# Kernel tuning notes

Hardware: AMD Instinct MI355X
Metric: run time of the kernel (lower is better)

The kernel has to match this reference:

```python
import jax, jax.numpy as jnp
import numpy as np

NUM_CUSTOMERS = 300000
NUM_PRODUCTS = 150000
NUM_GROUPS = 2000
NUM_BRANDS = 500
EMB_DIM = 64
NUM_LAYERS = 3


def setup_inputs() -> dict:
    key = jax.random.key(0)
    ks = jax.random.split(key, 20)
    def ri(k, n, hi):
        return jax.random.randint(k, (n,), 0, hi, dtype=jnp.int32)
    return {
        'cust_w': 0.1 * jax.random.normal(ks[0], (NUM_CUSTOMERS, EMB_DIM), jnp.float32),
        'prod_w': 0.1 * jax.random.normal(ks[1], (NUM_PRODUCTS, EMB_DIM), jnp.float32),
        'group_w': 0.1 * jax.random.normal(ks[2], (NUM_GROUPS, EMB_DIM), jnp.float32),
        'brand_w': 0.1 * jax.random.normal(ks[3], (NUM_BRANDS, EMB_DIM), jnp.float32),
        'purch_src': ri(ks[4], 2000000, NUM_CUSTOMERS),
        'purch_dst': ri(ks[5], 2000000, NUM_PRODUCTS),
        'pby_src': ri(ks[6], 2000000, NUM_PRODUCTS),
        'pby_dst': ri(ks[7], 2000000, NUM_CUSTOMERS),
        'sim_src': ri(ks[8], 500000, NUM_PRODUCTS),
        'sim_dst': ri(ks[9], 500000, NUM_PRODUCTS),
        'cop_src': ri(ks[10], 1000000, NUM_PRODUCTS),
        'cop_dst': ri(ks[11], 1000000, NUM_PRODUCTS),
        'bel_src': ri(ks[12], 150000, NUM_PRODUCTS),
        'bel_dst': ri(ks[13], 150000, NUM_GROUPS),
        'comp_src': ri(ks[14], 300000, NUM_PRODUCTS),
        'comp_dst': ri(ks[15], 300000, NUM_BRANDS),
    }


def _propagate(src_idx, tgt_idx, tgt_emb, n_src):
    # gather target embeddings along edges, scatter-add into source buckets,
    # normalize by source out-degree (clamped to >= 1) -- LightGCN mean-agg.
    msg = tgt_emb[tgt_idx]                                    # [E, D]
    agg = jax.ops.segment_sum(msg, src_idx, num_segments=n_src)
    cnt = jax.ops.segment_sum(jnp.ones(src_idx.shape, tgt_emb.dtype),
                              src_idx, num_segments=n_src)
    return agg / jnp.maximum(cnt, 1.0)[:, None]


def reference(cust_w, prod_w, group_w, brand_w,
              purch_src, purch_dst, pby_src, pby_dst,
              sim_src, sim_dst, cop_src, cop_dst,
              bel_src, bel_dst, comp_src, comp_dst):
    customer_emb, product_emb = cust_w, prod_w
    group_emb, brand_emb = group_w, brand_w
    customer_embs = [customer_emb]
    product_embs = [product_emb]
    for _ in range(NUM_LAYERS):
        customer_to_product = _propagate(purch_src, purch_dst, product_emb, NUM_CUSTOMERS)
        product_agg = product_emb
        product_agg = product_agg + _propagate(pby_src, pby_dst, customer_emb, NUM_PRODUCTS)
        product_agg = product_agg + 0.5 * _propagate(sim_src, sim_dst, product_emb, NUM_PRODUCTS)
        product_agg = product_agg + 0.3 * _propagate(cop_src, cop_dst, product_emb, NUM_PRODUCTS)
        product_agg = product_agg + 0.2 * _propagate(bel_src, bel_dst, group_emb, NUM_PRODUCTS)
        product_agg = product_agg + 0.2 * _propagate(comp_src, comp_dst, brand_emb, NUM_PRODUCTS)
        customer_emb = customer_to_product
        product_emb = product_agg
        customer_embs.append(customer_emb)
        product_embs.append(product_emb)
    final_customer = jnp.mean(jnp.stack(customer_embs, 0), axis=0)
    final_product = jnp.mean(jnp.stack(product_embs, 0), axis=0)
    # group/brand embeddings are never updated -> mean of identical copies
    return (final_customer, final_product, group_emb, brand_emb)
```

## Files before the change

kernel.cpp:

```cpp
#include <hip/hip_runtime.h>

#define NC 300000
#define NP 150000
#define NG 2000
#define NB 500
#define SCAN_B 1024
#define BK_SHIFT 11
#define BK_KEYS 2048
#define NBKT 513
#define CH 8192

typedef unsigned int u32;
typedef float  f32x4 __attribute__((ext_vector_type(4)));
typedef unsigned int u32x4 __attribute__((ext_vector_type(4)));

static inline unsigned cdiv(long long a, long long b) { return (unsigned)((a + b - 1) / b); }

__device__ __forceinline__ float b2f(u32 h) {
    union { u32 u; float f; } c; c.u = h << 16; return c.f;
}
__device__ __forceinline__ u32 f2b(float f) {
    union { float f; u32 u; } c; c.f = f;
    return (c.u + 0x7FFFu + ((c.u >> 16) & 1u)) >> 16;
}
__device__ __forceinline__ void unpack8(uint4 v, float* o) {
    o[0] = b2f(v.x & 0xFFFFu); o[1] = b2f(v.x >> 16);
    o[2] = b2f(v.y & 0xFFFFu); o[3] = b2f(v.y >> 16);
    o[4] = b2f(v.z & 0xFFFFu); o[5] = b2f(v.z >> 16);
    o[6] = b2f(v.w & 0xFFFFu); o[7] = b2f(v.w >> 16);
}
__device__ __forceinline__ void unpack8v(u32x4 v, float* o) {
    o[0] = b2f(v.x & 0xFFFFu); o[1] = b2f(v.x >> 16);
    o[2] = b2f(v.y & 0xFFFFu); o[3] = b2f(v.y >> 16);
    o[4] = b2f(v.z & 0xFFFFu); o[5] = b2f(v.z >> 16);
    o[6] = b2f(v.w & 0xFFFFu); o[7] = b2f(v.w >> 16);
}
__device__ __forceinline__ uint4 pack8(const float* a) {
    uint4 v;
    v.x = f2b(a[0]) | (f2b(a[1]) << 16);
    v.y = f2b(a[2]) | (f2b(a[3]) << 16);
    v.z = f2b(a[4]) | (f2b(a[5]) << 16);
    v.w = f2b(a[6]) | (f2b(a[7]) << 16);
    return v;
}

__global__ void convert_all(const float* __restrict__ cw, const float* __restrict__ pw,
                            const float* __restrict__ gw, const float* __restrict__ bw,
                            uint4* __restrict__ c16, uint4* __restrict__ p16,
                            uint4* __restrict__ g16, uint4* __restrict__ b16,
                            float* __restrict__ outg, float* __restrict__ outb) {
    const int C8 = NC * 8, P8 = NP * 8, G8 = NG * 8, B8 = NB * 8;
    int i = blockIdx.x * blockDim.x + threadIdx.x;
    const float* in; uint4* out16; float* cpy = nullptr; int j;
    if (i < C8)                         { in = cw; out16 = c16; j = i; }
    else if ((j = i - C8) < P8)         { in = pw; out16 = p16; }
    else if ((j = i - C8 - P8) < G8)    { in = gw; out16 = g16; cpy = outg; }
    else if ((j = i - C8 - P8 - G8) < B8){ in = bw; out16 = b16; cpy = outb; }
    else return;
    const float4* p = (const float4*)(in + (size_t)j * 8);
    float4 a = p[0], b = p[1];
    float t[8] = { a.x, a.y, a.z, a.w, b.x, b.y, b.z, b.w };
    out16[j] = pack8(t);
    if (cpy) { float4* q = (float4*)(cpy + (size_t)j * 8); q[0] = a; q[1] = b; }
}

struct Edges6 {
    const int* src[6];
    const int* dst[6];
    int cum[7];
    int ctbase[7];
};

__global__ void bcount(Edges6 e, int* __restrict__ gcount, int total) {
    __shared__ int hist[NBKT];
    int t = threadIdx.x;
    int j0 = blockIdx.x * CH;
    for (int b = t; b < NBKT; b += blockDim.x) hist[b] = 0;
    __syncthreads();
    #pragma unroll 4
    for (int q = 0; q < CH / 256; ++q) {
        int j = j0 + q * 256 + t;
        if (j < total) {
            int k = 0;
            #pragma unroll
            for (int qq = 1; qq < 6; ++qq) k += (j >= e.cum[qq]);
            int key = e.ctbase[k] + __builtin_nontemporal_load(e.src[k] + (j - e.cum[k]));
            atomicAdd(&hist[key >> BK_SHIFT], 1);
        }
    }
    __syncthreads();
    for (int b = t; b < NBKT; b += blockDim.x) {
        int c = hist[b];
        if (c > 0) atomicAdd(gcount + b, c);
    }
}

__global__ void bscan(const int* __restrict__ gcount, int* __restrict__ gbase,
                      int* __restrict__ gcur, int nb) {
    __shared__ int sm[SCAN_B];
    int t = threadIdx.x;
    int v = (t < nb) ? gcount[t] : 0;
    sm[t] = v; __syncthreads();
    for (int off = 1; off < SCAN_B; off <<= 1) {
        int add = (t >= off) ? sm[t - off] : 0;
        __syncthreads();
        sm[t] += add; __syncthreads();
    }
    int excl = sm[t] - v;
    if (t < nb) { gbase[t] = excl; gcur[t] = excl; }
    if (t == nb - 1) gbase[nb] = sm[t];
}

__global__ void msplit(Edges6 e, int* __restrict__ gcur, u32* __restrict__ stage, int total) {
    __shared__ int hist[NBKT];
    __shared__ int bse[NBKT];
    int t = threadIdx.x;
    int j0 = blockIdx.x * CH;
    for (int b = t; b < NBKT; b += blockDim.x) hist[b] = 0;
    __syncthreads();
    #pragma unroll 4
    for (int q = 0; q < CH / 256; ++q) {
        int j = j0 + q * 256 + t;
        if (j < total) {
            int k = 0;
            #pragma unroll
            for (int qq = 1; qq < 6; ++qq) k += (j >= e.cum[qq]);
            int key = e.ctbase[k] + __builtin_nontemporal_load(e.src[k] + (j - e.cum[k]));
            atomicAdd(&hist[key >> BK_SHIFT], 1);
        }
    }
    __syncthreads();
    for (int b = t; b < NBKT; b += blockDim.x) {
        int c = hist[b];
        bse[b] = (c > 0) ? atomicAdd(gcur + b, c) : 0;
        hist[b] = 0;
    }
    __syncthreads();
    #pragma unroll 4
    for (int q = 0; q < CH / 256; ++q) {
        int j = j0 + q * 256 + t;
        if (j < total) {
            int k = 0;
            #pragma unroll
            for (int qq = 1; qq < 6; ++qq) k += (j >= e.cum[qq]);
            int jj = j - e.cum[k];
            int key = e.ctbase[k] + __builtin_nontemporal_load(e.src[k] + jj);
            int d = __builtin_nontemporal_load(e.dst[k] + jj);
            int b = key >> BK_SHIFT;
            int off = atomicAdd(&hist[b], 1);
            stage[bse[b] + off] = ((u32)(key & (BK_KEYS - 1)) << 19) | (u32)d;
        }
    }
}

__global__ void sortb(const int* __restrict__ gbase, const u32* __restrict__ stage,
                      int* __restrict__ pm, int* __restrict__ rp, int rtot) {
    __shared__ int cur[BK_KEYS];
    __shared__ int part[512];
    int b = blockIdx.x, t = threadIdx.x;
    int k0 = b << BK_SHIFT;
    int base = gbase[b], end = gbase[b + 1];
    for (int q = t; q < BK_KEYS; q += 512) cur[q] = 0;
    __syncthreads();
    for (int i = base + t; i < end; i += 512)
        atomicAdd(&cur[stage[i] >> 19], 1);
    __syncthreads();
    int a0 = cur[4 * t], a1 = cur[4 * t + 1], a2 = cur[4 * t + 2], a3 = cur[4 * t + 3];
    int s = a0 + a1 + a2 + a3;
    part[t] = s; __syncthreads();
    for (int off = 1; off < 512; off <<= 1) {
        int add = (t >= off) ? part[t - off] : 0;
        __syncthreads();
        part[t] += add; __syncthreads();
    }
    int c0 = base + part[t] - s;
    int c1 = c0 + a0, c2 = c1 + a1, c3 = c2 + a2;
    cur[4 * t] = c0; cur[4 * t + 1] = c1; cur[4 * t + 2] = c2; cur[4 * t + 3] = c3;
    int ki = k0 + 4 * t;
    if (ki + 3 < rtot) {
        *(int4*)(rp + ki) = make_int4(c0, c1, c2, c3);
    } else {
        if (ki     < rtot) rp[ki]     = c0;
        if (ki + 1 < rtot) rp[ki + 1] = c1;
        if (ki + 2 < rtot) rp[ki + 2] = c2;
        if (ki + 3 < rtot) rp[ki + 3] = c3;
    }
    __syncthreads();
    for (int i = base + t; i < end; i += 512) {
        u32 w = stage[i];
        int off = atomicAdd(&cur[w >> 19], 1);
        pm[off] = (int)(w & 0x7FFFFu);
    }
}

__device__ __forceinline__ void acc8(uint4 v, float* sum) {
    float t[8]; unpack8(v, t);
    #pragma unroll
    for (int k = 0; k < 8; ++k) sum[k] += t[k];
}
__device__ __forceinline__ void agg8se(int s, int e, const int* __restrict__ pm,
                                       const uint4* __restrict__ tgt,
                                       int lane, float w, float* acc) {
    float sum[8] = {0, 0, 0, 0, 0, 0, 0, 0};
    int i = s;
    for (; i + 4 <= e; i += 4) {
        int d0 = __builtin_nontemporal_load(pm + i);
        int d1 = __builtin_nontemporal_load(pm + i + 1);
        int d2 = __builtin_nontemporal_load(pm + i + 2);
        int d3 = __builtin_nontemporal_load(pm + i + 3);
        uint4 v0 = tgt[(size_t)d0 * 8 + lane];
        uint4 v1 = tgt[(size_t)d1 * 8 + lane];
        uint4 v2 = tgt[(size_t)d2 * 8 + lane];
        uint4 v3 = tgt[(size_t)d3 * 8 + lane];
        acc8(v0, sum); acc8(v1, sum); acc8(v2, sum); acc8(v3, sum);
    }
    for (; i < e; ++i) {
        int d = __builtin_nontemporal_load(pm + i);
        uint4 v = tgt[(size_t)d * 8 + lane];
        acc8(v, sum);
    }
    int deg = e - s;
    float sc = w / (float)(deg > 1 ? deg : 1);
    #pragma unroll
    for (int k = 0; k < 8; ++k) acc[k] += sum[k] * sc;
}

__global__ void layer_kernel(
    const int* __restrict__ rp_purch, const int* __restrict__ rp_pby,
    const int* __restrict__ rp_sim,   const int* __restrict__ rp_cop,
    const int* __restrict__ rp_bel,   const int* __restrict__ rp_comp,
    const int* __restrict__ pm,
    const uint4* __restrict__ c16, const uint4* __restrict__ p16,
    const uint4* __restrict__ g16, const uint4* __restrict__ b16,
    uint4* __restrict__ c16n, uint4* __restrict__ p16n,
    const float* __restrict__ cw, const float* __restrict__ pw,
    const uint4* __restrict__ s1c, const uint4* __restrict__ s1p,
    float* __restrict__ outc, float* __restrict__ outp,
    int mode)
{
    int t = blockIdx.x * blockDim.x + threadIdx.x;
    int gid = t >> 3;
    int lane = t & 7;
    float acc[8];
    if (gid < NP) {
        int row = gid;
        size_t idx = (size_t)row * 8 + lane;
        int s0 = rp_pby[row],  e0 = rp_pby[row + 1];
        int s1 = rp_sim[row],  e1 = rp_sim[row + 1];
        int s2 = rp_cop[row],  e2 = rp_cop[row + 1];
        int s3 = rp_bel[row],  e3 = rp_bel[row + 1];
        int s4 = rp_comp[row], e4 = rp_comp[row + 1];
        float base[8]; unpack8(p16[idx], base);
        #pragma unroll
        for (int k = 0; k < 8; ++k) acc[k] = base[k];
        agg8se(s0, e0, pm, c16, lane, 1.0f, acc);
        agg8se(s1, e1, pm, p16, lane, 0.5f, acc);
        agg8se(s2, e2, pm, p16, lane, 0.3f, acc);
        agg8se(s3, e3, pm, g16, lane, 0.2f, acc);
        agg8se(s4, e4, pm, b16, lane, 0.2f, acc);
        if (mode != 2) {
            p16n[idx] = pack8(acc);
        } else {
            const f32x4* s0p = (const f32x4*)(pw + (size_t)row * 64 + lane * 8);
            f32x4 a0 = __builtin_nontemporal_load(s0p);
            f32x4 a1 = __builtin_nontemporal_load(s0p + 1);
            u32x4 s1v = __builtin_nontemporal_load((const u32x4*)&s1p[idx]);
            float sv[8]; unpack8v(s1v, sv);
            f32x4 o0, o1;
            o0.x = 0.25f * (a0.x + sv[0] + base[0] + acc[0]);
            o0.y = 0.25f * (a0.y + sv[1] + base[1] + acc[1]);
            o0.z = 0.25f * (a0.z + sv[2] + base[2] + acc[2]);
            o0.w = 0.25f * (a0.w + sv[3] + base[3] + acc[3]);
            o1.x = 0.25f * (a1.x + sv[4] + base[4] + acc[4]);
            o1.y = 0.25f * (a1.y + sv[5] + base[5] + acc[5]);
            o1.z = 0.25f * (a1.z + sv[6] + base[6] + acc[6]);
            o1.w = 0.25f * (a1.w + sv[7] + base[7] + acc[7]);
            f32x4* o = (f32x4*)(outp + (size_t)row * 64 + lane * 8);
            __builtin_nontemporal_store(o0, o);
            __builtin_nontemporal_store(o1, o + 1);
        }
    } else if (gid < NP + NC) {
        int row = gid - NP;
        size_t idx = (size_t)row * 8 + lane;
        int s0 = rp_purch[row], e0 = rp_purch[row + 1];
        #pragma unroll
        for (int k = 0; k < 8; ++k) acc[k] = 0.f;
        agg8se(s0, e0, pm, p16, lane, 1.0f, acc);
        if (mode != 2) {
            c16n[idx] = pack8(acc);
        } else {
            float base[8]; unpack8(c16[idx], base);
            const f32x4* s0c = (const f32x4*)(cw + (size_t)row * 64 + lane * 8);
            f32x4 a0 = __builtin_nontemporal_load(s0c);
            f32x4 a1 = __builtin_nontemporal_load(s0c + 1);
            u32x4 s1v = __builtin_nontemporal_load((const u32x4*)&s1c[idx]);
            float sv[8]; unpack8v(s1v, sv);
            f32x4 o0, o1;
            o0.x = 0.25f * (a0.x + sv[0] + base[0] + acc[0]);
            o0.y = 0.25f * (a0.y + sv[1] + base[1] + acc[1]);
            o0.z = 0.25f * (a0.z + sv[2] + base[2] + acc[2]);
            o0.w = 0.25f * (a0.w + sv[3] + base[3] + acc[3]);
            o1.x = 0.25f * (a1.x + sv[4] + base[4] + acc[4]);
            o1.y = 0.25f * (a1.y + sv[5] + base[5] + acc[5]);
            o1.z = 0.25f * (a1.z + sv[6] + base[6] + acc[6]);
            o1.w = 0.25f * (a1.w + sv[7] + base[7] + acc[7]);
            f32x4* o = (f32x4*)(outc + (size_t)row * 64 + lane * 8);
            __builtin_nontemporal_store(o0, o);
            __builtin_nontemporal_store(o1, o + 1);
        }
    }
}

extern "C" void kernel_launch(void* const* d_in, const int* in_sizes, int n_in,
                              void* d_out, int out_size, void* d_ws, size_t ws_size,
                              hipStream_t stream) {
    const float* cust_w  = (const float*)d_in[0];
    const float* prod_w  = (const float*)d_in[1];
    const float* group_w = (const float*)d_in[2];
    const float* brand_w = (const float*)d_in[3];

    const int n_purch = in_sizes[4];
    const int n_pby   = in_sizes[6];
    const int n_sim   = in_sizes[8];
    const int n_cop   = in_sizes[10];
    const int n_bel   = in_sizes[12];
    const int n_comp  = in_sizes[14];
    const int n_edges[6] = { n_purch, n_pby, n_sim, n_cop, n_bel, n_comp };

    const size_t CSZ = (size_t)NC * 64;
    const size_t PSZ = (size_t)NP * 64;

    char* base = (char*)d_ws;
    uint4* c16A = (uint4*)base;                 base += (size_t)NC * 128;
    uint4* c16B = (uint4*)base;                 base += (size_t)NC * 128;
    uint4* p16A = (uint4*)base;                 base += (size_t)NP * 128;
    uint4* p16B = (uint4*)base;                 base += (size_t)NP * 128;
    uint4* g16  = (uint4*)base;                 base += (size_t)NG * 128;
    uint4* b16  = (uint4*)base;                 base += (size_t)NB * 128;

    const int RP_PURCH = NC + 1;
    const int RP_OTHER = NP + 1;
    const int RTOT = RP_PURCH + 5 * RP_OTHER;

    int* rp_all = (int*)base;                   base += (size_t)RTOT * 4;
    long long tot_edges = 0;
    for (int k = 0; k < 6; ++k) tot_edges += n_edges[k];
    int* pm_all = (int*)base;                   base += tot_edges * 4;
    u32* stage  = (u32*)base;                   base += tot_edges * 4;
    int* gcount = (int*)base;                   base += (size_t)NBKT * 4;
    int* gbase  = (int*)base;                   base += (size_t)(NBKT + 1) * 4;
    int* gcur   = (int*)base;

    int* rp_purch = rp_all;
    int* rp_pby   = rp_purch + RP_PURCH;
    int* rp_sim   = rp_pby + RP_OTHER;
    int* rp_cop   = rp_sim + RP_OTHER;
    int* rp_bel   = rp_cop + RP_OTHER;
    int* rp_comp  = rp_bel + RP_OTHER;

    float* out_c = (float*)d_out;
    float* out_p = out_c + CSZ;
    float* out_g = out_p + PSZ;
    float* out_b = out_g + (size_t)NG * 64;

    const int BT = 256;

    const long long CVT = (long long)(NC + NP + NG + NB) * 8;
    convert_all<<<cdiv(CVT, BT), BT, 0, stream>>>(
        cust_w, prod_w, group_w, brand_w, c16A, p16A, g16, b16, out_g, out_b);

    Edges6 E;
    E.src[0] = (const int*)d_in[4];  E.dst[0] = (const int*)d_in[5];
    E.src[1] = (const int*)d_in[6];  E.dst[1] = (const int*)d_in[7];
    E.src[2] = (const int*)d_in[8];  E.dst[2] = (const int*)d_in[9];
    E.src[3] = (const int*)d_in[10]; E.dst[3] = (const int*)d_in[11];
    E.src[4] = (const int*)d_in[12]; E.dst[4] = (const int*)d_in[13];
    E.src[5] = (const int*)d_in[14]; E.dst[5] = (const int*)d_in[15];
    E.cum[0] = 0;
    for (int k = 0; k < 6; ++k) E.cum[k + 1] = E.cum[k] + n_edges[k];
    E.ctbase[0] = 0;
    E.ctbase[1] = RP_PURCH;
    for (int k = 2; k < 6; ++k) E.ctbase[k] = E.ctbase[k - 1] + RP_OTHER;
    E.ctbase[6] = RTOT;
    const int TOT = E.cum[6];

    hipMemsetAsync(gcount, 0, (size_t)NBKT * 4, stream);
    bcount<<<cdiv(TOT, CH), BT, 0, stream>>>(E, gcount, TOT);
    bscan<<<1, SCAN_B, 0, stream>>>(gcount, gbase, gcur, NBKT);
    msplit<<<cdiv(TOT, CH), BT, 0, stream>>>(E, gcur, stage, TOT);
    sortb<<<NBKT, 512, 0, stream>>>(gbase, stage, pm_all, rp_all, RTOT);

    const long long LTHREADS = (long long)(NP + NC) * 8;
    layer_kernel<<<cdiv(LTHREADS, BT), BT, 0, stream>>>(
        rp_purch, rp_pby, rp_sim, rp_cop, rp_bel, rp_comp, pm_all,
        c16A, p16A, g16, b16, c16B, p16B,
        cust_w, prod_w, c16B, p16B, out_c, out_p, 0);
    layer_kernel<<<cdiv(LTHREADS, BT), BT, 0, stream>>>(
        rp_purch, rp_pby, rp_sim, rp_cop, rp_bel, rp_comp, pm_all,
        c16B, p16B, g16, b16, c16A, p16A,
        cust_w, prod_w, c16B, p16B, out_c, out_p, 1);
    layer_kernel<<<cdiv(LTHREADS, BT), BT, 0, stream>>>(
        rp_purch, rp_pby, rp_sim, rp_cop, rp_bel, rp_comp, pm_all,
        c16A, p16A, g16, b16, c16B, p16B,
        cust_w, prod_w, c16B, p16B,
        out_c, out_p, 2);
}
```

Measured before the change: 728.2 us.

## Sort rows by degree bin and pack CSR offsets for load-balanced layer kernel

Adds a preprocessing pass (histogram, scan, placement) that groups product and customer rows by total degree. It then precomputes packed per-row start/end offsets in that permuted order. The layer kernel walks rows in degree-sorted order, so neighbouring 8-lane groups within a wavefront have similar loop trip counts, which should reduce divergence and tail imbalance. The cost is four extra kernels and extra memory traffic. Output rows are now written in scattered order, which may hurt store and base-row locality. The index loads in the aggregation loop also switch from nontemporal to ordinary loads.

```diff
diff --git a/kernel.cpp b/kernel.cpp
--- a/kernel.cpp
+++ b/kernel.cpp
@@ -9,6 +9,8 @@
 #define BK_KEYS 2048
 #define NBKT 513
 #define CH 8192
+#define ROWS (NP + NC)
+#define RCH 4096
 
 typedef unsigned int u32;
 typedef float  f32x4 __attribute__((ext_vector_type(4)));
@@ -193,6 +195,98 @@
     }
 }
 
+__device__ __forceinline__ int row_bin(const int* __restrict__ rp, int gid) {
+    if (gid < NP) {
+        int td = 0;
+        #pragma unroll
+        for (int k = 0; k < 5; ++k) {
+            int o = (NC + 1) + k * (NP + 1) + gid;
+            td += rp[o + 1] - rp[o];
+        }
+        return td < 127 ? td : 127;
+    } else {
+        int r = gid - NP;
+        int d = rp[r + 1] - rp[r];
+        return 128 + (d < 127 ? d : 127);
+    }
+}
+
+__global__ void rowhist(const int* __restrict__ rp, int* __restrict__ gbinc, int rows) {
+    __shared__ int hist[256];
+    int t = threadIdx.x;
+    hist[t] = 0;
+    __syncthreads();
+    int j0 = blockIdx.x * RCH;
+    for (int q = 0; q < RCH / 256; ++q) {
+        int j = j0 + q * 256 + t;
+        if (j < rows) atomicAdd(&hist[row_bin(rp, j)], 1);
+    }
+    __syncthreads();
+    int c = hist[t];
+    if (c > 0) atomicAdd(gbinc + t, c);
+}
+
+__global__ void rowscan(const int* __restrict__ gbinc, int* __restrict__ gcur256) {
+    __shared__ int sm[256];
+    int t = threadIdx.x;
+    int v = gbinc[t];
+    sm[t] = v; __syncthreads();
+    for (int off = 1; off < 256; off <<= 1) {
+        int add = (t >= off) ? sm[t - off] : 0;
+        __syncthreads();
+        sm[t] += add; __syncthreads();
+    }
+    gcur256[t] = sm[t] - v;
+}
+
+__global__ void rowplace(const int* __restrict__ rp, int* __restrict__ gcur256,
+                         int* __restrict__ perm, int rows) {
+    __shared__ int hist[256];
+    __shared__ int bse[256];
+    int t = threadIdx.x;
+    hist[t] = 0;
+    __syncthreads();
+    int j0 = blockIdx.x * RCH;
+    for (int q = 0; q < RCH / 256; ++q) {
+        int j = j0 + q * 256 + t;
+        if (j < rows) atomicAdd(&hist[row_bin(rp, j)], 1);
+    }
+    __syncthreads();
+    int c = hist[t];
+    bse[t] = (c > 0) ? atomicAdd(gcur256 + t, c) : 0;
+    hist[t] = 0;
+    __syncthreads();
+    for (int q = 0; q < RCH / 256; ++q) {
+        int j = j0 + q * 256 + t;
+        if (j < rows) {
+            int b = row_bin(rp, j);
+            int off = atomicAdd(&hist[b], 1);
+            perm[bse[b] + off] = j;
+        }
+    }
+}
+
+__global__ void permrp(const int* __restrict__ rp, const int* __restrict__ perm,
+                       int4* __restrict__ pA, int4* __restrict__ pB, int2* __restrict__ pC,
+                       int2* __restrict__ cinfo, int rows) {
+    int j = blockIdx.x * blockDim.x + threadIdx.x;
+    if (j >= rows) return;
+    int pg = perm[j];
+    if (pg < NP) {
+        const int* r0 = rp + (NC + 1) + pg;
+        const int* r1 = r0 + (NP + 1);
+        const int* r2 = r1 + (NP + 1);
+        const int* r3 = r2 + (NP + 1);
+        const int* r4 = r3 + (NP + 1);
+        pA[j] = make_int4(r0[0], r0[1], r1[0], r1[1]);
+        pB[j] = make_int4(r2[0], r2[1], r3[0], r3[1]);
+        pC[j] = make_int2(r4[0], r4[1]);
+    } else {
+        int r = pg - NP;
+        cinfo[j - NP] = make_int2(rp[r], rp[r + 1]);
+    }
+}
+
 __device__ __forceinline__ void acc8(uint4 v, float* sum) {
     float t[8]; unpack8(v, t);
     #pragma unroll
@@ -204,10 +298,7 @@
     float sum[8] = {0, 0, 0, 0, 0, 0, 0, 0};
     int i = s;
     for (; i + 4 <= e; i += 4) {
-        int d0 = __builtin_nontemporal_load(pm + i);
-        int d1 = __builtin_nontemporal_load(pm + i + 1);
-        int d2 = __builtin_nontemporal_load(pm + i + 2);
-        int d3 = __builtin_nontemporal_load(pm + i + 3);
+        int d0 = pm[i], d1 = pm[i + 1], d2 = pm[i + 2], d3 = pm[i + 3];
         uint4 v0 = tgt[(size_t)d0 * 8 + lane];
         uint4 v1 = tgt[(size_t)d1 * 8 + lane];
         uint4 v2 = tgt[(size_t)d2 * 8 + lane];
@@ -215,8 +306,7 @@
         acc8(v0, sum); acc8(v1, sum); acc8(v2, sum); acc8(v3, sum);
     }
     for (; i < e; ++i) {
-        int d = __builtin_nontemporal_load(pm + i);
-        uint4 v = tgt[(size_t)d * 8 + lane];
+        uint4 v = tgt[(size_t)pm[i] * 8 + lane];
         acc8(v, sum);
     }
     int deg = e - s;
@@ -226,9 +316,9 @@
 }
 
 __global__ void layer_kernel(
-    const int* __restrict__ rp_purch, const int* __restrict__ rp_pby,
-    const int* __restrict__ rp_sim,   const int* __restrict__ rp_cop,
-    const int* __restrict__ rp_bel,   const int* __restrict__ rp_comp,
+    const int* __restrict__ perm,
+    const int4* __restrict__ pA, const int4* __restrict__ pB, const int2* __restrict__ pC,
+    const int2* __restrict__ cinfo,
     const int* __restrict__ pm,
     const uint4* __restrict__ c16, const uint4* __restrict__ p16,
     const uint4* __restrict__ g16, const uint4* __restrict__ b16,
@@ -243,21 +333,19 @@
     int lane = t & 7;
     float acc[8];
     if (gid < NP) {
-        int row = gid;
+        int row = perm[gid];
         size_t idx = (size_t)row * 8 + lane;
-        int s0 = rp_pby[row],  e0 = rp_pby[row + 1];
-        int s1 = rp_sim[row],  e1 = rp_sim[row + 1];
-        int s2 = rp_cop[row],  e2 = rp_cop[row + 1];
-        int s3 = rp_bel[row],  e3 = rp_bel[row + 1];
-        int s4 = rp_comp[row], e4 = rp_comp[row + 1];
+        int4 ia = pA[gid];
+        int4 ib = pB[gid];
+        int2 ic = pC[gid];
         float base[8]; unpack8(p16[idx], base);
         #pragma unroll
         for (int k = 0; k < 8; ++k) acc[k] = base[k];
-        agg8se(s0, e0, pm, c16, lane, 1.0f, acc);
-        agg8se(s1, e1, pm, p16, lane, 0.5f, acc);
-        agg8se(s2, e2, pm, p16, lane, 0.3f, acc);
-        agg8se(s3, e3, pm, g16, lane, 0.2f, acc);
-        agg8se(s4, e4, pm, b16, lane, 0.2f, acc);
+        agg8se(ia.x, ia.y, pm, c16, lane, 1.0f, acc);
+        agg8se(ia.z, ia.w, pm, p16, lane, 0.5f, acc);
+        agg8se(ib.x, ib.y, pm, p16, lane, 0.3f, acc);
+        agg8se(ib.z, ib.w, pm, g16, lane, 0.2f, acc);
+        agg8se(ic.x, ic.y, pm, b16, lane, 0.2f, acc);
         if (mode != 2) {
             p16n[idx] = pack8(acc);
         } else {
@@ -279,13 +367,13 @@
             __builtin_nontemporal_store(o0, o);
             __builtin_nontemporal_store(o1, o + 1);
         }
-    } else if (gid < NP + NC) {
-        int row = gid - NP;
+    } else if (gid < ROWS) {
+        int row = perm[gid] - NP;
         size_t idx = (size_t)row * 8 + lane;
-        int s0 = rp_purch[row], e0 = rp_purch[row + 1];
+        int2 se = cinfo[gid - NP];
         #pragma unroll
         for (int k = 0; k < 8; ++k) acc[k] = 0.f;
-        agg8se(s0, e0, pm, p16, lane, 1.0f, acc);
+        agg8se(se.x, se.y, pm, p16, lane, 1.0f, acc);
         if (mode != 2) {
             c16n[idx] = pack8(acc);
         } else {
@@ -349,14 +437,14 @@
     u32* stage  = (u32*)base;                   base += tot_edges * 4;
     int* gcount = (int*)base;                   base += (size_t)NBKT * 4;
     int* gbase  = (int*)base;                   base += (size_t)(NBKT + 1) * 4;
-    int* gcur   = (int*)base;
-
-    int* rp_purch = rp_all;
-    int* rp_pby   = rp_purch + RP_PURCH;
-    int* rp_sim   = rp_pby + RP_OTHER;
-    int* rp_cop   = rp_sim + RP_OTHER;
-    int* rp_bel   = rp_cop + RP_OTHER;
-    int* rp_comp  = rp_bel + RP_OTHER;
+    int* gcur   = (int*)base;                   base += (size_t)NBKT * 4;
+    int* gbinc  = (int*)base;                   base += 256 * 4;
+    int* gcur256= (int*)base;                   base += 256 * 4;
+    int* perm   = (int*)base;                   base += (size_t)ROWS * 4;
+    int4* pA    = (int4*)base;                  base += (size_t)NP * 16;
+    int4* pB    = (int4*)base;                  base += (size_t)NP * 16;
+    int2* pC    = (int2*)base;                  base += (size_t)NP * 8;
+    int2* cinfo = (int2*)base;                  base += (size_t)NC * 8;
 
     float* out_c = (float*)d_out;
     float* out_p = out_c + CSZ;
@@ -385,22 +473,28 @@
     const int TOT = E.cum[6];
 
     hipMemsetAsync(gcount, 0, (size_t)NBKT * 4, stream);
+    hipMemsetAsync(gbinc, 0, 256 * 4, stream);
     bcount<<<cdiv(TOT, CH), BT, 0, stream>>>(E, gcount, TOT);
     bscan<<<1, SCAN_B, 0, stream>>>(gcount, gbase, gcur, NBKT);
     msplit<<<cdiv(TOT, CH), BT, 0, stream>>>(E, gcur, stage, TOT);
     sortb<<<NBKT, 512, 0, stream>>>(gbase, stage, pm_all, rp_all, RTOT);
 
-    const long long LTHREADS = (long long)(NP + NC) * 8;
+    rowhist<<<cdiv(ROWS, RCH), 256, 0, stream>>>(rp_all, gbinc, ROWS);
+    rowscan<<<1, 256, 0, stream>>>(gbinc, gcur256);
+    rowplace<<<cdiv(ROWS, RCH), 256, 0, stream>>>(rp_all, gcur256, perm, ROWS);
+    permrp<<<cdiv(ROWS, BT), BT, 0, stream>>>(rp_all, perm, pA, pB, pC, cinfo, ROWS);
+
+    const long long LTHREADS = (long long)ROWS * 8;
     layer_kernel<<<cdiv(LTHREADS, BT), BT, 0, stream>>>(
-        rp_purch, rp_pby, rp_sim, rp_cop, rp_bel, rp_comp, pm_all,
+        perm, pA, pB, pC, cinfo, pm_all,
         c16A, p16A, g16, b16, c16B, p16B,
         cust_w, prod_w, c16B, p16B, out_c, out_p, 0);
     layer_kernel<<<cdiv(LTHREADS, BT), BT, 0, stream>>>(
-        rp_purch, rp_pby, rp_sim, rp_cop, rp_bel, rp_comp, pm_all,
+        perm, pA, pB, pC, cinfo, pm_all,
         c16B, p16B, g16, b16, c16A, p16A,
         cust_w, prod_w, c16B, p16B, out_c, out_p, 1);
     layer_kernel<<<cdiv(LTHREADS, BT), BT, 0, stream>>>(
-        rp_purch, rp_pby, rp_sim, rp_cop, rp_bel, rp_comp, pm_all,
+        perm, pA, pB, pC, cinfo, pm_all,
         c16A, p16A, g16, b16, c16B, p16B,
         cust_w, prod_w, c16B, p16B,
         out_c, out_p, 2);
```

New measurement: 670.7 us. 1.09x faster.
